# Performance work log

Measured on AMD Instinct MI355X. Metric: run time of the kernel, lower is better.

Reference implementation:

```python
import jax, jax.numpy as jnp
import numpy as np

INPUT_SZ = 1024
HIDDEN_SZ = 1024

def setup_inputs() -> dict:
    key = jax.random.key(0)
    k1, k2, k3 = jax.random.split(key, 3)
    x = jax.random.normal(k1, (64, 512, INPUT_SZ), dtype=jnp.float32)
    # nn.Linear(input_sz+hidden_sz, hidden_sz): weight [hidden, input+hidden], bias [hidden]
    bound = 1.0 / np.sqrt(INPUT_SZ + HIDDEN_SZ)
    W = jax.random.uniform(k2, (HIDDEN_SZ, INPUT_SZ + HIDDEN_SZ), dtype=jnp.float32, minval=-bound, maxval=bound)
    b = jax.random.uniform(k3, (HIDDEN_SZ,), dtype=jnp.float32, minval=-bound, maxval=bound)
    return {"x": x, "W": W, "b": b}

def reference(x, W, b):
    # Split the concat-linear into two contractions: [x_t, h_t] @ W.T = x_t @ Wx.T + h_t @ Wh.T
    Wx = W[:, :INPUT_SZ]   # [H, I]
    Wh = W[:, INPUT_SZ:]   # [H, H]
    B = x.shape[0]
    # Precompute the input projection for all timesteps in one big GEMM.
    xp = jnp.einsum('bti,hi->bth', x, Wx) + b  # [B, T, H]
    h0 = jnp.zeros((B, HIDDEN_SZ), dtype=x.dtype)

    def step(h, xp_t):
        h_new = jnp.tanh(xp_t + h @ Wh.T)
        return h_new, h_new

    _, hs = jax.lax.scan(step, h0, jnp.swapaxes(xp, 0, 1))  # hs: [T, B, H]
    return jnp.swapaxes(hs, 0, 1)  # [B, T, H]
```

## Files before the change

kernel.cpp:

```cpp
#include <hip/hip_runtime.h>


typedef unsigned short u16;
typedef unsigned u32;
typedef unsigned long long u64;
typedef __attribute__((ext_vector_type(4))) float f32x4;
typedef __attribute__((ext_vector_type(8))) short bf16x8;
typedef __attribute__((ext_vector_type(4))) u32 u32x4;

__device__ __forceinline__ u16 f2bf(float f) {
  unsigned u = __builtin_bit_cast(unsigned, f);
  unsigned r = (u + 0x7fffu + ((u >> 16) & 1u)) >> 16;
  return (u16)r;
}

__device__ __forceinline__ u16 f2bf_par(float f, unsigned bit) {
  unsigned rt = __builtin_bit_cast(unsigned, f) >> 16;
  return (u16)(((rt & 1u) == bit) ? rt : rt + 1u);
}

__device__ __forceinline__ float fast_tanh(float x) {
  float e = __expf(2.0f * x);
  return 1.0f - 2.0f / (e + 1.0f);
}

__device__ __forceinline__ void async_cp16(u16* lds, const u16* g) {
  __builtin_amdgcn_global_load_lds(
      (const __attribute__((address_space(1))) unsigned int*)g,
      (__attribute__((address_space(3))) unsigned int*)lds, 16, 0, 0);
}


__global__ __launch_bounds__(256) void conv_x_kernel(const float* __restrict__ in,
                                                     u16* __restrict__ outb) {
  const size_t i = (size_t)blockIdx.x * 256 + threadIdx.x;
  const float4* p = (const float4*)(in + (i << 3));
  float4 a = p[0], b = p[1];
  bf16x8 v;
  v[0] = (short)f2bf(a.x); v[1] = (short)f2bf(a.y);
  v[2] = (short)f2bf(a.z); v[3] = (short)f2bf(a.w);
  v[4] = (short)f2bf(b.x); v[5] = (short)f2bf(b.y);
  v[6] = (short)f2bf(b.z); v[7] = (short)f2bf(b.w);
  *(bf16x8*)(outb + (i << 3)) = v;
}

__global__ __launch_bounds__(256) void conv_w_kernel(const float* __restrict__ W,
                                                     u16* __restrict__ Wx,
                                                     u16* __restrict__ Wh) {
  const int i = blockIdx.x * 256 + threadIdx.x;
  const int j = i >> 8;
  const int c = (i & 255) << 3;
  const float4* p = (const float4*)(W + (size_t)j * 2048 + c);
  float4 a = p[0], b = p[1];
  bf16x8 v;
  v[0] = (short)f2bf(a.x); v[1] = (short)f2bf(a.y);
  v[2] = (short)f2bf(a.z); v[3] = (short)f2bf(a.w);
  v[4] = (short)f2bf(b.x); v[5] = (short)f2bf(b.y);
  v[6] = (short)f2bf(b.z); v[7] = (short)f2bf(b.w);
  u16* dst = (c < 1024) ? (Wx + (size_t)j * 1024 + c)
                        : (Wh + (size_t)j * 1024 + (c - 1024));
  *(bf16x8*)dst = v;
}


__global__ __launch_bounds__(256, 2) void gemm_xp(const u16* __restrict__ A,
                                                  const u16* __restrict__ B,
                                                  const float* __restrict__ bias,
                                                  float* __restrict__ C) {
  const int bid = blockIdx.x;
  const int swz = (bid & 7) * 256 + (bid >> 3);
  const int m0 = (swz >> 3) << 7;
  const int n0 = (swz & 7) << 7;
  const int tid = threadIdx.x;
  const int lane = tid & 63;
  const int wv = tid >> 6;
  const int mw = (wv >> 1) << 6;
  const int nw = (wv & 1) << 6;

  __shared__ __align__(16) u16 Alds[128 * 32];
  __shared__ __align__(16) u16 Blds[128 * 32];

  f32x4 acc[4][4] = {};

  for (int kt = 0; kt < 32; ++kt) {
    const int k0 = kt << 5;
#pragma unroll
    for (int i = 0; i < 2; ++i) {
      const int off = (i << 11) + (tid << 3);
      const int row = off >> 5;
      const int col = off & 31;
      async_cp16(&Alds[off], A + (size_t)(m0 + row) * 1024 + k0 + col);
      async_cp16(&Blds[off], B + (size_t)(n0 + row) * 1024 + k0 + col);
    }
    __syncthreads();
    bf16x8 af[4], bf[4];
#pragma unroll
    for (int mi = 0; mi < 4; ++mi)
      af[mi] = *(const bf16x8*)&Alds[((mw + (mi << 4) + (lane & 15)) << 5) +
                                     ((lane >> 4) << 3)];
#pragma unroll
    for (int ni = 0; ni < 4; ++ni)
      bf[ni] = *(const bf16x8*)&Blds[((nw + (ni << 4) + (lane & 15)) << 5) +
                                     ((lane >> 4) << 3)];
#pragma unroll
    for (int mi = 0; mi < 4; ++mi)
#pragma unroll
      for (int ni = 0; ni < 4; ++ni)
        acc[mi][ni] = __builtin_amdgcn_mfma_f32_16x16x32_bf16(
            af[mi], bf[ni], acc[mi][ni], 0, 0, 0);
    __syncthreads();
  }

  float bv[4];
#pragma unroll
  for (int ni = 0; ni < 4; ++ni)
    bv[ni] = bias[n0 + nw + (ni << 4) + (lane & 15)];
#pragma unroll
  for (int mi = 0; mi < 4; ++mi) {
#pragma unroll
    for (int r = 0; r < 4; ++r) {
      const int row = m0 + mw + (mi << 4) + ((lane >> 4) << 2) + r;
      float* cp = C + (size_t)row * 1024 + n0 + nw + (lane & 15);
#pragma unroll
      for (int ni = 0; ni < 4; ++ni) cp[ni << 4] = acc[mi][ni][r] + bv[ni];
    }
  }
}


__global__ __launch_bounds__(512, 1) void rnn_scan(float* __restrict__ out,
                                                   const u16* __restrict__ Wh,
                                                   char* __restrict__ Hb) {
  const int wg = blockIdx.x;
  const int g = wg & 3;
  const int wloc = wg >> 2;
  const int tid = threadIdx.x;
  const int lane = tid & 63;
  const int wv = tid >> 6;
  const int l16 = lane & 15;
  const int lhi = lane >> 4;

  __shared__ __align__(16) f32x4 red[2][8][4][64];

  bf16x8 af[4][4];
  {
    const u16* wp =
        Wh + (size_t)((wloc << 6) + l16) * 1024 + (wv << 7) + (lhi << 3);
#pragma unroll
    for (int jt = 0; jt < 4; ++jt)
#pragma unroll
      for (int kk = 0; kk < 4; ++kk)
        af[jt][kk] = *(const bf16x8*)(wp + (jt << 14) + (kk << 5));
  }

  const int b = (g << 4) + l16;
  const int hread = (g << 15) + (((wv << 4) + lhi) << 8) + (l16 << 4);
  const int wvp = wv & 3;
  const int jq = (wloc << 4) + (wvp << 2) + lhi;
  const int hwrite = (g << 15) + ((jq >> 1) << 8) + (l16 << 4) + ((jq & 1) << 3);
  const int j0 = jq << 2;
  const bool prod = (wv < 4);
  float* pout = out + ((size_t)b << 19) + j0;

  f32x4 xpA = {0.f, 0.f, 0.f, 0.f};
  f32x4 xpB = {0.f, 0.f, 0.f, 0.f};
  f32x4 hvP = {0.f, 0.f, 0.f, 0.f};
  if (prod) {
    xpA = __builtin_nontemporal_load((const f32x4*)pout);
    xpB = __builtin_nontemporal_load((const f32x4*)(pout + 1024));
  }

#pragma unroll 1
  for (int t = 0; t < 512; ++t) {
    f32x4 acc[4] = {};
    if (t > 0) {
      const u32 e = 1u + ((((u32)t - 1u) >> 1) & 1u);
      const char* Hs = Hb + (((t - 1) & 1) << 17) + hread;
      u32x4 f0, f1, f2, f3;
      while (true) {
        asm volatile(
            "global_load_dwordx4 %0, %4, off sc0 sc1\n\t"
            "global_load_dwordx4 %1, %4, off offset:1024 sc0 sc1\n\t"
            "global_load_dwordx4 %2, %4, off offset:2048 sc0 sc1\n\t"
            "global_load_dwordx4 %3, %4, off offset:3072 sc0 sc1\n\t"
            "s_waitcnt vmcnt(0)"
            : "=&v"(f0), "=&v"(f1), "=&v"(f2), "=&v"(f3)
            : "v"(Hs)
            : "memory");
        u32 ok = 1u;
#pragma unroll
        for (int d = 0; d < 4; ++d) {
          ok &= (u32)(((f0[d] & 1u) | (((f0[d] >> 16) & 1u) << 1)) == e);
          ok &= (u32)(((f1[d] & 1u) | (((f1[d] >> 16) & 1u) << 1)) == e);
          ok &= (u32)(((f2[d] & 1u) | (((f2[d] >> 16) & 1u) << 1)) == e);
          ok &= (u32)(((f3[d] & 1u) | (((f3[d] >> 16) & 1u) << 1)) == e);
        }
        if (__all((int)ok)) break;
      }
      if (prod)
        __builtin_nontemporal_store(hvP,
                                    (f32x4*)(pout + ((size_t)(t - 1) << 10)));
      union { u32x4 u; bf16x8 v; } c0, c1, c2, c3;
      c0.u = f0; c1.u = f1; c2.u = f2; c3.u = f3;
#pragma unroll
      for (int jt = 0; jt < 4; ++jt) {
        acc[jt] = __builtin_amdgcn_mfma_f32_16x16x32_bf16(af[jt][0], c0.v,
                                                          acc[jt], 0, 0, 0);
        acc[jt] = __builtin_amdgcn_mfma_f32_16x16x32_bf16(af[jt][1], c1.v,
                                                          acc[jt], 0, 0, 0);
        acc[jt] = __builtin_amdgcn_mfma_f32_16x16x32_bf16(af[jt][2], c2.v,
                                                          acc[jt], 0, 0, 0);
        acc[jt] = __builtin_amdgcn_mfma_f32_16x16x32_bf16(af[jt][3], c3.v,
                                                          acc[jt], 0, 0, 0);
      }
    }

    const int rb = t & 1;
#pragma unroll
    for (int jt = 0; jt < 4; ++jt) red[rb][wv][jt][lane] = acc[jt];
    asm volatile("s_waitcnt lgkmcnt(0)\n\ts_barrier" ::: "memory");

    if (prod) {
      f32x4 s = red[rb][0][wvp][lane];
#pragma unroll
      for (int w = 1; w < 8; ++w) s += red[rb][w][wvp][lane];

      const f32x4 xp = (t & 1) ? xpB : xpA;
      const float h0 = fast_tanh(xp[0] + s[0]);
      const float h1 = fast_tanh(xp[1] + s[1]);
      const float h2 = fast_tanh(xp[2] + s[2]);
      const float h3 = fast_tanh(xp[3] + s[3]);

      const u32 code = 1u + (((u32)t >> 1) & 1u);
      const u32 c0b = code & 1u, c1b = (code >> 1) & 1u;
      const u64 pack = (u64)f2bf_par(h0, c0b) | ((u64)f2bf_par(h1, c1b) << 16) |
                       ((u64)f2bf_par(h2, c0b) << 32) |
                       ((u64)f2bf_par(h3, c1b) << 48);
      __hip_atomic_store((u64*)(Hb + ((t & 1) << 17) + hwrite), pack,
                         __ATOMIC_RELAXED, __HIP_MEMORY_SCOPE_AGENT);

      if (t + 2 < 512) {
        const f32x4* src = (const f32x4*)(pout + ((size_t)(t + 2) << 10));
        if (t & 1)
          xpB = __builtin_nontemporal_load(src);
        else
          xpA = __builtin_nontemporal_load(src);
      }
      hvP[0] = h0; hvP[1] = h1; hvP[2] = h2; hvP[3] = h3;
    }
  }
  if (prod)
    __builtin_nontemporal_store(hvP, (f32x4*)(pout + ((size_t)511 << 10)));
}


extern "C" void kernel_launch(void* const* d_in, const int* in_sizes, int n_in,
                              void* d_out, int out_size, void* d_ws,
                              size_t ws_size, hipStream_t stream) {
  const float* x = (const float*)d_in[0];
  const float* W = (const float*)d_in[1];
  const float* bias = (const float*)d_in[2];
  float* out = (float*)d_out;

  char* ws = (char*)d_ws;
  u16* xb = (u16*)ws;
  u16* Wxb = (u16*)(ws + 67108864);
  u16* Whb = (u16*)(ws + 69206016);
  char* Hbuf = (char*)(ws + 71303168);

  (void)hipMemsetAsync(Hbuf, 0, 262144, stream);
  conv_x_kernel<<<16384, 256, 0, stream>>>(x, xb);
  conv_w_kernel<<<1024, 256, 0, stream>>>(W, Wxb, Whb);
  gemm_xp<<<2048, 256, 0, stream>>>(xb, Wxb, bias, out);
  rnn_scan<<<64, 512, 0, stream>>>(out, Whb, Hbuf);
}
```

Before: 1.120 ms.

## Halve scan workgroup to 4 waves with doubled K-slice per wave

The recurrent scan kernel moves from 8 waves per workgroup, each covering a 128-wide K slice, to 4 waves each covering a 256-wide K slice. Every wave now holds twice as many Wh fragments in registers, loads eight h chunks per step, and also acts as a producer. The cross-wave LDS reduction shrinks from 8 partials to 4 and no waves sit idle during the tanh/store phase. In exchange each wave runs twice as many MFMAs per step on the serial critical path, and register pressure goes up.

```diff
diff --git a/kernel.cpp b/kernel.cpp
--- a/kernel.cpp
+++ b/kernel.cpp
@@ -128,9 +128,9 @@
 }
 
 
-__global__ __launch_bounds__(512, 1) void rnn_scan(float* __restrict__ out,
-                                                   const u16* __restrict__ Wh,
-                                                   char* __restrict__ Hb) {
+__global__ __launch_bounds__(256) void rnn_scan(float* __restrict__ out,
+                                                const u16* __restrict__ Wh,
+                                                char* __restrict__ Hb) {
   const int wg = blockIdx.x;
   const int g = wg & 3;
   const int wloc = wg >> 2;
@@ -140,35 +140,29 @@
   const int l16 = lane & 15;
   const int lhi = lane >> 4;
 
-  __shared__ __align__(16) f32x4 red[2][8][4][64];
-
-  bf16x8 af[4][4];
+  __shared__ __align__(16) f32x4 red[2][4][4][64];
+
+  bf16x8 af[4][8];
   {
     const u16* wp =
-        Wh + (size_t)((wloc << 6) + l16) * 1024 + (wv << 7) + (lhi << 3);
+        Wh + (size_t)((wloc << 6) + l16) * 1024 + (wv << 8) + (lhi << 3);
 #pragma unroll
     for (int jt = 0; jt < 4; ++jt)
 #pragma unroll
-      for (int kk = 0; kk < 4; ++kk)
+      for (int kk = 0; kk < 8; ++kk)
         af[jt][kk] = *(const bf16x8*)(wp + (jt << 14) + (kk << 5));
   }
 
   const int b = (g << 4) + l16;
-  const int hread = (g << 15) + (((wv << 4) + lhi) << 8) + (l16 << 4);
-  const int wvp = wv & 3;
-  const int jq = (wloc << 4) + (wvp << 2) + lhi;
+  const int hread = (g << 15) + (((wv << 5) + lhi) << 8) + (l16 << 4);
+  const int jq = (wloc << 4) + (wv << 2) + lhi;
   const int hwrite = (g << 15) + ((jq >> 1) << 8) + (l16 << 4) + ((jq & 1) << 3);
   const int j0 = jq << 2;
-  const bool prod = (wv < 4);
   float* pout = out + ((size_t)b << 19) + j0;
 
-  f32x4 xpA = {0.f, 0.f, 0.f, 0.f};
-  f32x4 xpB = {0.f, 0.f, 0.f, 0.f};
+  f32x4 xpA = __builtin_nontemporal_load((const f32x4*)pout);
+  f32x4 xpB = __builtin_nontemporal_load((const f32x4*)(pout + 1024));
   f32x4 hvP = {0.f, 0.f, 0.f, 0.f};
-  if (prod) {
-    xpA = __builtin_nontemporal_load((const f32x4*)pout);
-    xpB = __builtin_nontemporal_load((const f32x4*)(pout + 1024));
-  }
 
 #pragma unroll 1
   for (int t = 0; t < 512; ++t) {
@@ -176,16 +170,22 @@
     if (t > 0) {
       const u32 e = 1u + ((((u32)t - 1u) >> 1) & 1u);
       const char* Hs = Hb + (((t - 1) & 1) << 17) + hread;
-      u32x4 f0, f1, f2, f3;
+      const char* Hs2 = Hs + 4096;
+      u32x4 f0, f1, f2, f3, f4, f5, f6, f7;
       while (true) {
         asm volatile(
-            "global_load_dwordx4 %0, %4, off sc0 sc1\n\t"
-            "global_load_dwordx4 %1, %4, off offset:1024 sc0 sc1\n\t"
-            "global_load_dwordx4 %2, %4, off offset:2048 sc0 sc1\n\t"
-            "global_load_dwordx4 %3, %4, off offset:3072 sc0 sc1\n\t"
+            "global_load_dwordx4 %0, %8, off sc0 sc1\n\t"
+            "global_load_dwordx4 %1, %8, off offset:1024 sc0 sc1\n\t"
+            "global_load_dwordx4 %2, %8, off offset:2048 sc0 sc1\n\t"
+            "global_load_dwordx4 %3, %8, off offset:3072 sc0 sc1\n\t"
+            "global_load_dwordx4 %4, %9, off sc0 sc1\n\t"
+            "global_load_dwordx4 %5, %9, off offset:1024 sc0 sc1\n\t"
+            "global_load_dwordx4 %6, %9, off offset:2048 sc0 sc1\n\t"
+            "global_load_dwordx4 %7, %9, off offset:3072 sc0 sc1\n\t"
             "s_waitcnt vmcnt(0)"
-            : "=&v"(f0), "=&v"(f1), "=&v"(f2), "=&v"(f3)
-            : "v"(Hs)
+            : "=&v"(f0), "=&v"(f1), "=&v"(f2), "=&v"(f3), "=&v"(f4),
+              "=&v"(f5), "=&v"(f6), "=&v"(f7)
+            : "v"(Hs), "v"(Hs2)
             : "memory");
         u32 ok = 1u;
 #pragma unroll
@@ -194,25 +194,24 @@
           ok &= (u32)(((f1[d] & 1u) | (((f1[d] >> 16) & 1u) << 1)) == e);
           ok &= (u32)(((f2[d] & 1u) | (((f2[d] >> 16) & 1u) << 1)) == e);
           ok &= (u32)(((f3[d] & 1u) | (((f3[d] >> 16) & 1u) << 1)) == e);
+          ok &= (u32)(((f4[d] & 1u) | (((f4[d] >> 16) & 1u) << 1)) == e);
+          ok &= (u32)(((f5[d] & 1u) | (((f5[d] >> 16) & 1u) << 1)) == e);
+          ok &= (u32)(((f6[d] & 1u) | (((f6[d] >> 16) & 1u) << 1)) == e);
+          ok &= (u32)(((f7[d] & 1u) | (((f7[d] >> 16) & 1u) << 1)) == e);
         }
         if (__all((int)ok)) break;
       }
-      if (prod)
-        __builtin_nontemporal_store(hvP,
-                                    (f32x4*)(pout + ((size_t)(t - 1) << 10)));
-      union { u32x4 u; bf16x8 v; } c0, c1, c2, c3;
-      c0.u = f0; c1.u = f1; c2.u = f2; c3.u = f3;
-#pragma unroll
-      for (int jt = 0; jt < 4; ++jt) {
-        acc[jt] = __builtin_amdgcn_mfma_f32_16x16x32_bf16(af[jt][0], c0.v,
-                                                          acc[jt], 0, 0, 0);
-        acc[jt] = __builtin_amdgcn_mfma_f32_16x16x32_bf16(af[jt][1], c1.v,
-                                                          acc[jt], 0, 0, 0);
-        acc[jt] = __builtin_amdgcn_mfma_f32_16x16x32_bf16(af[jt][2], c2.v,
-                                                          acc[jt], 0, 0, 0);
-        acc[jt] = __builtin_amdgcn_mfma_f32_16x16x32_bf16(af[jt][3], c3.v,
-                                                          acc[jt], 0, 0, 0);
-      }
+      __builtin_nontemporal_store(hvP,
+                                  (f32x4*)(pout + ((size_t)(t - 1) << 10)));
+      union { u32x4 u; bf16x8 v; } c[8];
+      c[0].u = f0; c[1].u = f1; c[2].u = f2; c[3].u = f3;
+      c[4].u = f4; c[5].u = f5; c[6].u = f6; c[7].u = f7;
+#pragma unroll
+      for (int kk = 0; kk < 8; ++kk)
+#pragma unroll
+        for (int jt = 0; jt < 4; ++jt)
+          acc[jt] = __builtin_amdgcn_mfma_f32_16x16x32_bf16(af[jt][kk], c[kk].v,
+                                                            acc[jt], 0, 0, 0);
     }
 
     const int rb = t & 1;
@@ -220,37 +219,34 @@
     for (int jt = 0; jt < 4; ++jt) red[rb][wv][jt][lane] = acc[jt];
     asm volatile("s_waitcnt lgkmcnt(0)\n\ts_barrier" ::: "memory");
 
-    if (prod) {
-      f32x4 s = red[rb][0][wvp][lane];
-#pragma unroll
-      for (int w = 1; w < 8; ++w) s += red[rb][w][wvp][lane];
-
-      const f32x4 xp = (t & 1) ? xpB : xpA;
-      const float h0 = fast_tanh(xp[0] + s[0]);
-      const float h1 = fast_tanh(xp[1] + s[1]);
-      const float h2 = fast_tanh(xp[2] + s[2]);
-      const float h3 = fast_tanh(xp[3] + s[3]);
-
-      const u32 code = 1u + (((u32)t >> 1) & 1u);
-      const u32 c0b = code & 1u, c1b = (code >> 1) & 1u;
-      const u64 pack = (u64)f2bf_par(h0, c0b) | ((u64)f2bf_par(h1, c1b) << 16) |
-                       ((u64)f2bf_par(h2, c0b) << 32) |
-                       ((u64)f2bf_par(h3, c1b) << 48);
-      __hip_atomic_store((u64*)(Hb + ((t & 1) << 17) + hwrite), pack,
-                         __ATOMIC_RELAXED, __HIP_MEMORY_SCOPE_AGENT);
-
-      if (t + 2 < 512) {
-        const f32x4* src = (const f32x4*)(pout + ((size_t)(t + 2) << 10));
-        if (t & 1)
-          xpB = __builtin_nontemporal_load(src);
-        else
-          xpA = __builtin_nontemporal_load(src);
-      }
-      hvP[0] = h0; hvP[1] = h1; hvP[2] = h2; hvP[3] = h3;
-    }
-  }
-  if (prod)
-    __builtin_nontemporal_store(hvP, (f32x4*)(pout + ((size_t)511 << 10)));
+    f32x4 s = red[rb][0][wv][lane];
+#pragma unroll
+    for (int w = 1; w < 4; ++w) s += red[rb][w][wv][lane];
+
+    const f32x4 xp = (t & 1) ? xpB : xpA;
+    const float h0 = fast_tanh(xp[0] + s[0]);
+    const float h1 = fast_tanh(xp[1] + s[1]);
+    const float h2 = fast_tanh(xp[2] + s[2]);
+    const float h3 = fast_tanh(xp[3] + s[3]);
+
+    const u32 code = 1u + (((u32)t >> 1) & 1u);
+    const u32 c0b = code & 1u, c1b = (code >> 1) & 1u;
+    const u64 pack = (u64)f2bf_par(h0, c0b) | ((u64)f2bf_par(h1, c1b) << 16) |
+                     ((u64)f2bf_par(h2, c0b) << 32) |
+                     ((u64)f2bf_par(h3, c1b) << 48);
+    __hip_atomic_store((u64*)(Hb + ((t & 1) << 17) + hwrite), pack,
+                       __ATOMIC_RELAXED, __HIP_MEMORY_SCOPE_AGENT);
+
+    if (t + 2 < 512) {
+      const f32x4* src = (const f32x4*)(pout + ((size_t)(t + 2) << 10));
+      if (t & 1)
+        xpB = __builtin_nontemporal_load(src);
+      else
+        xpA = __builtin_nontemporal_load(src);
+    }
+    hvP[0] = h0; hvP[1] = h1; hvP[2] = h2; hvP[3] = h3;
+  }
+  __builtin_nontemporal_store(hvP, (f32x4*)(pout + ((size_t)511 << 10)));
 }
 
 
@@ -272,5 +268,5 @@
   conv_x_kernel<<<16384, 256, 0, stream>>>(x, xb);
   conv_w_kernel<<<1024, 256, 0, stream>>>(W, Wxb, Whb);
   gemm_xp<<<2048, 256, 0, stream>>>(xb, Wxb, bias, out);
-  rnn_scan<<<64, 512, 0, stream>>>(out, Whb, Hbuf);
-}
+  rnn_scan<<<64, 256, 0, stream>>>(out, Whb, Hbuf);
+}
```

Result: faster. 1.053 ms (-6.0%).
